# Optimization experiments

Hardware: AMD Instinct MI355X
Metric: run time of the kernel (lower is better)

Reference implementation:

```python
import jax, jax.numpy as jnp
import numpy as np

EPS = 1e-6
NEG_SLOPE = 0.2


def knn_idx(xf, k):
    # xf: (B, C, N) flattened vector features; returns (B, N, k) neighbor indices
    xx = jnp.sum(xf * xf, axis=1)                       # (B, N)
    inner = jnp.einsum('bcn,bcm->bnm', xf, xf)          # (B, N, N)
    neg_dist = 2.0 * inner - xx[:, :, None] - xx[:, None, :]  # -||xi-xj||^2
    _, idx = jax.lax.top_k(neg_dist, k)                 # includes self (dist 0)
    return idx


def get_graph_feature(x, k):
    # x: (B, D, 3, N) -> edge features (B, 2D, 3, N, k)
    B, D, _, N = x.shape
    idx = knn_idx(x.reshape(B, D * 3, N), k)            # (B, N, k)
    pts = jnp.transpose(x, (0, 3, 1, 2))                # (B, N, D, 3)
    neigh = jax.vmap(lambda p, i: p[i])(pts, idx)       # (B, N, k, D, 3) gather
    center = jnp.broadcast_to(pts[:, :, None], neigh.shape)
    feat = jnp.concatenate([neigh - center, center], axis=3)  # (B, N, k, 2D, 3)
    return jnp.transpose(feat, (0, 3, 4, 1, 2))


def vn_linear_leakyrelu(x, Wf, Wd):
    # Vector-Neuron linear + leaky ReLU. x: (B, Cin, 3, ...),
    # Wf: (Cout, Cin), Wd: (Cout, Cin) or (1, Cin) when nonlinearity is shared.
    p = jnp.einsum('oi,bi...->bo...', Wf, x)
    d = jnp.einsum('oi,bi...->bo...', Wd, x)
    dot = jnp.sum(p * d, axis=2, keepdims=True)
    dsq = jnp.sum(d * d, axis=2, keepdims=True)
    proj = p - (dot / (dsq + EPS)) * d
    return NEG_SLOPE * p + (1.0 - NEG_SLOPE) * jnp.where(dot >= 0, p, proj)


def setup_inputs() -> dict:
    key = jax.random.key(0)
    ks = jax.random.split(key, 11)
    B, N = 8, 1024
    x = jax.random.normal(ks[0], (B, 3, N), dtype=jnp.float32)
    # dims = [1, 21, 21, 42, 85, 341]
    ins = [2, 42, 42, 84, 169]      # 2*dim_in for edge layers; sum(dims[1:-1]) for last
    outs = [21, 21, 42, 85, 341]
    dirs = [21, 21, 42, 85, 1]      # last layer has share_nonlinearity=True
    d = {"x": x}
    for i, (ci, co, cd) in enumerate(zip(ins, outs, dirs)):
        s = 1.0 / np.sqrt(ci)
        kf, kd = jax.random.split(ks[1 + i])
        d[f"Wf{i}"] = (jax.random.normal(kf, (co, ci), dtype=jnp.float32) * s)
        d[f"Wd{i}"] = (jax.random.normal(kd, (cd, ci), dtype=jnp.float32) * s)
    d["k"] = 20
    return d


def reference(x, Wf0, Wd0, Wf1, Wd1, Wf2, Wd2, Wf3, Wd3, Wf4, Wd4, k):
    cur = x[:, None]                 # (B, 1, 3, N)
    feats = []
    for Wf, Wd in ((Wf0, Wd0), (Wf1, Wd1), (Wf2, Wd2), (Wf3, Wd3)):
        g = get_graph_feature(cur, k)        # (B, 2D, 3, N, k)
        h = vn_linear_leakyrelu(g, Wf, Wd)   # (B, Dout, 3, N, k)
        cur = h.mean(axis=-1)                # mean over neighbors -> (B, Dout, 3, N)
        feats.append(cur)
    xcat = jnp.concatenate(feats, axis=1)    # (B, 169, 3, N)
    out = vn_linear_leakyrelu(xcat, Wf4, Wd4)
    return out.mean(axis=-1)                 # mean over points -> (B, 341, 3)
```

## Files before the change

kernel.cpp:

```cpp
#include <hip/hip_runtime.h>
#include <cstddef>

#define BB 8
#define NN 1024
#define KK 20
#define CCAT 169
#define NT 16

__global__ __launch_bounds__(256) void dist_tile_kernel(
    const float* __restrict__ src, int bs, int F, float* __restrict__ dist) {
  __shared__ float As[8][128];
  __shared__ float Bs[8][128];
  int b = blockIdx.z;
  int n0 = blockIdx.y * 128;
  int m0 = blockIdx.x * 128;
  int t = threadIdx.x;
  int tx = t & 15, ty = t >> 4;
  const float* p = src + (size_t)b * bs;

  float acc[8][8];
  float xn[8], xm[8];
#pragma unroll
  for (int i = 0; i < 8; ++i) {
    xn[i] = 0.f;
    xm[i] = 0.f;
#pragma unroll
    for (int j = 0; j < 8; ++j) acc[i][j] = 0.f;
  }

  int fr = t >> 5;
  int cc = (t & 31) << 2;
  for (int f0 = 0; f0 < F; f0 += 8) {
    int f = f0 + fr;
    float4 av = {0.f, 0.f, 0.f, 0.f}, bv = {0.f, 0.f, 0.f, 0.f};
    if (f < F) {
      av = *(const float4*)(p + (size_t)f * NN + n0 + cc);
      bv = *(const float4*)(p + (size_t)f * NN + m0 + cc);
    }
    __syncthreads();
    *(float4*)&As[fr][cc] = av;
    *(float4*)&Bs[fr][cc] = bv;
    __syncthreads();
#pragma unroll
    for (int f2 = 0; f2 < 8; ++f2) {
      float4 al = *(const float4*)&As[f2][ty << 2];
      float4 ah = *(const float4*)&As[f2][64 + (ty << 2)];
      float4 bl = *(const float4*)&Bs[f2][tx << 2];
      float4 bh = *(const float4*)&Bs[f2][64 + (tx << 2)];
      float a[8] = {al.x, al.y, al.z, al.w, ah.x, ah.y, ah.z, ah.w};
      float bb[8] = {bl.x, bl.y, bl.z, bl.w, bh.x, bh.y, bh.z, bh.w};
#pragma unroll
      for (int i = 0; i < 8; ++i) xn[i] += a[i] * a[i];
#pragma unroll
      for (int j = 0; j < 8; ++j) xm[j] += bb[j] * bb[j];
#pragma unroll
      for (int i = 0; i < 8; ++i)
#pragma unroll
        for (int j = 0; j < 8; ++j) acc[i][j] += a[i] * bb[j];
    }
  }

#pragma unroll
  for (int i = 0; i < 8; ++i) {
    int n = n0 + ((i < 4) ? ((ty << 2) + i) : (64 + (ty << 2) + i - 4));
    float* dr = dist + (((size_t)b * NN + n) << 10);
    float4 w0, w1;
    w0.x = 2.f * acc[i][0] - xn[i] - xm[0];
    w0.y = 2.f * acc[i][1] - xn[i] - xm[1];
    w0.z = 2.f * acc[i][2] - xn[i] - xm[2];
    w0.w = 2.f * acc[i][3] - xn[i] - xm[3];
    w1.x = 2.f * acc[i][4] - xn[i] - xm[4];
    w1.y = 2.f * acc[i][5] - xn[i] - xm[5];
    w1.z = 2.f * acc[i][6] - xn[i] - xm[6];
    w1.w = 2.f * acc[i][7] - xn[i] - xm[7];
    *(float4*)(dr + m0 + (tx << 2)) = w0;
    *(float4*)(dr + m0 + 64 + (tx << 2)) = w1;
  }
}

__device__ __forceinline__ unsigned long long shfl_xor_u64(
    unsigned long long v, int off) {
  unsigned lo = (unsigned)v, hi = (unsigned)(v >> 32);
  lo = __shfl_xor(lo, off, 64);
  hi = __shfl_xor(hi, off, 64);
  return ((unsigned long long)hi << 32) | lo;
}

__global__ __launch_bounds__(256) void topk_kernel(
    const float* __restrict__ dist, int* __restrict__ idx_out) {
  int wave = threadIdx.x >> 6;
  int lane = threadIdx.x & 63;
  int row = blockIdx.x * 4 + wave;
  const float* d = dist + ((size_t)row << 10);

  unsigned long long key[16];
#pragma unroll
  for (int s = 0; s < 16; ++s) {
    int m = lane + (s << 6);
    unsigned u = __float_as_uint(d[m]);
    u = (u & 0x80000000u) ? ~u : (u | 0x80000000u);
    key[s] = ((unsigned long long)u << 32) | (unsigned)(NN - 1 - m);
  }

#pragma unroll
  for (int size = 2; size <= 16; size <<= 1) {
#pragma unroll
    for (int stride = size >> 1; stride > 0; stride >>= 1) {
#pragma unroll
      for (int i = 0; i < 16; ++i) {
        int j = i ^ stride;
        if (j > i) {
          unsigned long long a = key[i], c = key[j];
          bool desc = ((i & size) == 0);
          bool sw = desc ? (a < c) : (a > c);
          key[i] = sw ? c : a;
          key[j] = sw ? a : c;
        }
      }
    }
  }

  int* out = idx_out + row * KK;
  unsigned long long head = key[0];
  for (int r = 0; r < KK; ++r) {
    unsigned long long w = head;
#pragma unroll
    for (int off = 32; off > 0; off >>= 1) {
      unsigned long long o = shfl_xor_u64(w, off);
      if (o > w) w = o;
    }
    if (lane == 0) out[r] = (NN - 1) - (int)(w & 0xFFFFFFFFull);
    if (head == w) {
#pragma unroll
      for (int s = 0; s < 15; ++s) key[s] = key[s + 1];
      key[15] = 0ull;
      head = key[0];
    }
  }
}

__global__ __launch_bounds__(256) void edge_fused_kernel(
    const float* __restrict__ src, int bs, int D, int Co,
    const float* __restrict__ Wf, const float* __restrict__ Wd,
    const int* __restrict__ idx, int ooff, float* __restrict__ xcat) {
  __shared__ float2 Ulds[3 * NN];
  __shared__ float2 Vlds[3 * NN];
  __shared__ float4 Wlds[48];
  int bo = blockIdx.x;
  int b = bo / Co, o = bo % Co;
  int t = threadIdx.x;

  if (t < D) {
    float wfa = Wf[o * 2 * D + t];
    float wfb = Wf[o * 2 * D + D + t] - wfa;
    float wda = Wd[o * 2 * D + t];
    float wdb = Wd[o * 2 * D + D + t] - wda;
    Wlds[t] = make_float4(wfa, wfb, wda, wdb);
  }
  __syncthreads();

  const float* sb = src + (size_t)b * bs;
#pragma unroll
  for (int r = 0; r < 3; ++r) {
    int g = t + 256 * r;
    float4 uf = {0.f, 0.f, 0.f, 0.f}, vf = {0.f, 0.f, 0.f, 0.f};
    float4 ud = {0.f, 0.f, 0.f, 0.f}, vd = {0.f, 0.f, 0.f, 0.f};
    for (int i = 0; i < D; ++i) {
      float4 s = *(const float4*)(sb + (size_t)i * 3 * NN + (g << 2));
      float4 w = Wlds[i];
      uf.x += w.x * s.x; uf.y += w.x * s.y; uf.z += w.x * s.z; uf.w += w.x * s.w;
      vf.x += w.y * s.x; vf.y += w.y * s.y; vf.z += w.y * s.z; vf.w += w.y * s.w;
      ud.x += w.z * s.x; ud.y += w.z * s.y; ud.z += w.z * s.z; ud.w += w.z * s.w;
      vd.x += w.w * s.x; vd.y += w.w * s.y; vd.z += w.w * s.z; vd.w += w.w * s.w;
    }
    *(float4*)&Ulds[(g << 2) + 0] = make_float4(uf.x, ud.x, uf.y, ud.y);
    *(float4*)&Ulds[(g << 2) + 2] = make_float4(uf.z, ud.z, uf.w, ud.w);
    *(float4*)&Vlds[(g << 2) + 0] = make_float4(vf.x, vd.x, vf.y, vd.y);
    *(float4*)&Vlds[(g << 2) + 2] = make_float4(vf.z, vd.z, vf.w, vd.w);
  }
  __syncthreads();

  const float inv_k = 1.f / KK;
#pragma unroll
  for (int rep = 0; rep < 4; ++rep) {
    int n = rep * 256 + t;
    float2 v0 = Vlds[n];
    float2 v1 = Vlds[NN + n];
    float2 v2 = Vlds[2 * NN + n];
    const int4* ip = (const int4*)(idx + (b * NN + n) * KK);
    float a0 = 0.f, a1 = 0.f, a2 = 0.f;
#pragma unroll
    for (int q = 0; q < 5; ++q) {
      int4 iv = ip[q];
      int nbs[4] = {iv.x, iv.y, iv.z, iv.w};
#pragma unroll
      for (int jj = 0; jj < 4; ++jj) {
        int nb = nbs[jj];
        float2 u0 = Ulds[nb];
        float2 u1 = Ulds[NN + nb];
        float2 u2 = Ulds[2 * NN + nb];
        float pf0 = u0.x + v0.x, pd0 = u0.y + v0.y;
        float pf1 = u1.x + v1.x, pd1 = u1.y + v1.y;
        float pf2 = u2.x + v2.x, pd2 = u2.y + v2.y;
        float dot = pf0 * pd0 + pf1 * pd1 + pf2 * pd2;
        float dsq = pd0 * pd0 + pd1 * pd1 + pd2 * pd2;
        float g = (dot >= 0.f) ? 0.f : 0.8f * dot / (dsq + 1e-6f);
        a0 += pf0 - g * pd0;
        a1 += pf1 - g * pd1;
        a2 += pf2 - g * pd2;
      }
    }
    size_t ob = (size_t)b * CCAT * 3 * NN + (size_t)(ooff + o) * 3 * NN + n;
    xcat[ob] = a0 * inv_k;
    xcat[ob + NN] = a1 * inv_k;
    xcat[ob + 2 * NN] = a2 * inv_k;
  }
}

__global__ __launch_bounds__(256) void final_fused_kernel(
    const float* __restrict__ xcat, const float* __restrict__ Wf4,
    const float* __restrict__ Wd4, float* __restrict__ part) {
  __shared__ float Ws[2][16][64];
  __shared__ float Xs[2][3][16][64];
  __shared__ float Wds[2][16];
  int b = blockIdx.z;
  int o0 = blockIdx.y * 64;
  int n0 = blockIdx.x * 64;
  int t = threadIdx.x;
  int tx = t & 15, ty = t >> 4;
  int ow = t & 63, fq = t >> 6;

  float acc[3][4][4];
  float dv[3][4];
#pragma unroll
  for (int c = 0; c < 3; ++c) {
#pragma unroll
    for (int i = 0; i < 4; ++i)
#pragma unroll
      for (int j = 0; j < 4; ++j) acc[c][i][j] = 0.f;
#pragma unroll
    for (int j = 0; j < 4; ++j) dv[c][j] = 0.f;
  }

  const float* xb = xcat + (size_t)b * CCAT * 3 * NN;
  const int NTILE = (CCAT + 15) / 16;

  float4 xv[3];
  float wreg[4];
  float wdv;

  auto stage = [&](int tt) {
    int f = tt * 16 + ty;
#pragma unroll
    for (int c = 0; c < 3; ++c) {
      xv[c] = make_float4(0.f, 0.f, 0.f, 0.f);
      if (f < CCAT)
        xv[c] = *(const float4*)(xb + ((size_t)f * 3 + c) * NN + n0 + (tx << 2));
    }
    int o = o0 + ow;
#pragma unroll
    for (int e = 0; e < 4; ++e) {
      int fw = tt * 16 + (fq << 2) + e;
      wreg[e] = (o < 341 && fw < CCAT) ? Wf4[(size_t)o * CCAT + fw] : 0.f;
    }
    wdv = 0.f;
    if (t < 16) {
      int fd = tt * 16 + t;
      if (fd < CCAT) wdv = Wd4[fd];
    }
  };
  auto store = [&](int buf) {
#pragma unroll
    for (int c = 0; c < 3; ++c) *(float4*)&Xs[buf][c][ty][tx << 2] = xv[c];
#pragma unroll
    for (int e = 0; e < 4; ++e) Ws[buf][(fq << 2) + e][ow] = wreg[e];
    if (t < 16) Wds[buf][t] = wdv;
  };

  stage(0);
  store(0);

  for (int tt = 0; tt < NTILE; ++tt) {
    int buf = tt & 1;
    __syncthreads();
    if (tt + 1 < NTILE) stage(tt + 1);
#pragma unroll
    for (int f2 = 0; f2 < 16; ++f2) {
      float4 w = *(const float4*)&Ws[buf][f2][ty << 2];
      float wa[4] = {w.x, w.y, w.z, w.w};
      float wd = Wds[buf][f2];
#pragma unroll
      for (int c = 0; c < 3; ++c) {
        float4 x = *(const float4*)&Xs[buf][c][f2][tx << 2];
        float xa[4] = {x.x, x.y, x.z, x.w};
#pragma unroll
        for (int j = 0; j < 4; ++j) dv[c][j] += wd * xa[j];
#pragma unroll
        for (int i = 0; i < 4; ++i)
#pragma unroll
          for (int j = 0; j < 4; ++j) acc[c][i][j] += wa[i] * xa[j];
      }
    }
    if (tt + 1 < NTILE) store(buf ^ 1);
  }

  float s[3][4];
#pragma unroll
  for (int c = 0; c < 3; ++c)
#pragma unroll
    for (int i = 0; i < 4; ++i) s[c][i] = 0.f;
#pragma unroll
  for (int i = 0; i < 4; ++i) {
#pragma unroll
    for (int j = 0; j < 4; ++j) {
      float d0 = dv[0][j], d1 = dv[1][j], d2 = dv[2][j];
      float p0 = acc[0][i][j], p1 = acc[1][i][j], p2 = acc[2][i][j];
      float dot = p0 * d0 + p1 * d1 + p2 * d2;
      float dsq = d0 * d0 + d1 * d1 + d2 * d2;
      float g = (dot >= 0.f) ? 0.f : 0.8f * dot / (dsq + 1e-6f);
      s[0][i] += p0 - g * d0;
      s[1][i] += p1 - g * d1;
      s[2][i] += p2 - g * d2;
    }
  }

#pragma unroll
  for (int off = 1; off < 16; off <<= 1) {
#pragma unroll
    for (int c = 0; c < 3; ++c)
#pragma unroll
      for (int i = 0; i < 4; ++i) s[c][i] += __shfl_xor(s[c][i], off, 64);
  }
  if (tx == 0) {
#pragma unroll
    for (int i = 0; i < 4; ++i) {
      int o = o0 + (ty << 2) + i;
      if (o < 341) {
#pragma unroll
        for (int c = 0; c < 3; ++c)
          part[(((size_t)b * 341 + o) * 3 + c) * NT + blockIdx.x] = s[c][i];
      }
    }
  }
}

__global__ void final_reduce_kernel(const float* __restrict__ part,
                                    float* __restrict__ out) {
  int t = blockIdx.x * 256 + threadIdx.x;
  if (t >= BB * 341 * 3) return;
  const float* p = part + (size_t)t * NT;
  float s = 0.f;
#pragma unroll
  for (int nt = 0; nt < NT; ++nt) s += p[nt];
  out[t] = s * (1.f / 1024.f);
}

extern "C" void kernel_launch(void* const* d_in, const int* in_sizes, int n_in,
                              void* d_out, int out_size, void* d_ws,
                              size_t ws_size, hipStream_t stream) {
  (void)in_sizes; (void)n_in; (void)out_size; (void)ws_size;
  const float* x = (const float*)d_in[0];
  const float* Wf[5] = {(const float*)d_in[1], (const float*)d_in[3],
                        (const float*)d_in[5], (const float*)d_in[7],
                        (const float*)d_in[9]};
  const float* Wd[5] = {(const float*)d_in[2], (const float*)d_in[4],
                        (const float*)d_in[6], (const float*)d_in[8],
                        (const float*)d_in[10]};

  float* ws = (float*)d_ws;
  float* dist = ws;
  float* part = ws;
  size_t off = (size_t)BB * NN * NN;
  int* idx = (int*)(ws + off);
  off += (size_t)BB * NN * KK;
  float* xcat = ws + off;

  struct LayerCfg { int D, Co, inoff, ooff; };
  const LayerCfg L[4] = {
      {1, 21, 0, 0},
      {21, 21, 0, 21},
      {21, 42, 21, 42},
      {42, 85, 42, 84},
  };

  for (int l = 0; l < 4; ++l) {
    const float* src = (l == 0) ? x : (xcat + (size_t)L[l].inoff * 3 * NN);
    int bs = (l == 0) ? 3 * NN : CCAT * 3 * NN;
    int D = L[l].D, Co = L[l].Co;

    dist_tile_kernel<<<dim3(8, 8, BB), 256, 0, stream>>>(src, bs, 3 * D, dist);
    topk_kernel<<<(BB * NN) / 4, 256, 0, stream>>>(dist, idx);
    edge_fused_kernel<<<BB * Co, 256, 0, stream>>>(src, bs, D, Co, Wf[l],
                                                   Wd[l], idx, L[l].ooff,
                                                   xcat);
  }

  final_fused_kernel<<<dim3(NT, 6, BB), 256, 0, stream>>>(xcat, Wf[4], Wd[4],
                                                          part);
  final_reduce_kernel<<<(BB * 341 * 3 + 255) / 256, 256, 0, stream>>>(
      part, (float*)d_out);
}
```

Baseline: 467.5 us.

## Exploit distance matrix symmetry and restructure final layer tiling

The distance kernel now computes only upper-triangular 128x128 tiles (36 of 64 per batch) and writes each off-diagonal tile twice, once transposed, which removes nearly half of the Gram-matrix arithmetic. The transposed stores are strided per thread and so less coalesced. The final fused kernel replaces register double-buffering with a 32-wide single-buffered tile and preloads Wd4 into shared memory once. It also reorganises the Wf4 loads so each thread fetches four outputs for one feature.

```diff
diff --git a/kernel.cpp b/kernel.cpp
--- a/kernel.cpp
+++ b/kernel.cpp
@@ -12,8 +12,11 @@
   __shared__ float As[8][128];
   __shared__ float Bs[8][128];
   int b = blockIdx.z;
-  int n0 = blockIdx.y * 128;
-  int m0 = blockIdx.x * 128;
+  int rem = blockIdx.x, bi = 0;
+  while (rem >= 8 - bi) { rem -= 8 - bi; ++bi; }
+  int bj = bi + rem;
+  int n0 = bi * 128;
+  int m0 = bj * 128;
   int t = threadIdx.x;
   int tx = t & 15, ty = t >> 4;
   const float* p = src + (size_t)b * bs;
@@ -61,20 +64,30 @@
   }
 
 #pragma unroll
+  for (int i = 0; i < 8; ++i)
+#pragma unroll
+    for (int j = 0; j < 8; ++j) acc[i][j] = 2.f * acc[i][j] - xn[i] - xm[j];
+
+#pragma unroll
   for (int i = 0; i < 8; ++i) {
     int n = n0 + ((i < 4) ? ((ty << 2) + i) : (64 + (ty << 2) + i - 4));
     float* dr = dist + (((size_t)b * NN + n) << 10);
-    float4 w0, w1;
-    w0.x = 2.f * acc[i][0] - xn[i] - xm[0];
-    w0.y = 2.f * acc[i][1] - xn[i] - xm[1];
-    w0.z = 2.f * acc[i][2] - xn[i] - xm[2];
-    w0.w = 2.f * acc[i][3] - xn[i] - xm[3];
-    w1.x = 2.f * acc[i][4] - xn[i] - xm[4];
-    w1.y = 2.f * acc[i][5] - xn[i] - xm[5];
-    w1.z = 2.f * acc[i][6] - xn[i] - xm[6];
-    w1.w = 2.f * acc[i][7] - xn[i] - xm[7];
-    *(float4*)(dr + m0 + (tx << 2)) = w0;
-    *(float4*)(dr + m0 + 64 + (tx << 2)) = w1;
+    *(float4*)(dr + m0 + (tx << 2)) =
+        make_float4(acc[i][0], acc[i][1], acc[i][2], acc[i][3]);
+    *(float4*)(dr + m0 + 64 + (tx << 2)) =
+        make_float4(acc[i][4], acc[i][5], acc[i][6], acc[i][7]);
+  }
+
+  if (bi != bj) {
+#pragma unroll
+    for (int j = 0; j < 8; ++j) {
+      int m = m0 + ((j < 4) ? ((tx << 2) + j) : (64 + (tx << 2) + j - 4));
+      float* dr = dist + (((size_t)b * NN + m) << 10);
+      *(float4*)(dr + n0 + (ty << 2)) =
+          make_float4(acc[0][j], acc[1][j], acc[2][j], acc[3][j]);
+      *(float4*)(dr + n0 + 64 + (ty << 2)) =
+          make_float4(acc[4][j], acc[5][j], acc[6][j], acc[7][j]);
+    }
   }
 }
 
@@ -220,15 +233,16 @@
 __global__ __launch_bounds__(256) void final_fused_kernel(
     const float* __restrict__ xcat, const float* __restrict__ Wf4,
     const float* __restrict__ Wd4, float* __restrict__ part) {
-  __shared__ float Ws[2][16][64];
-  __shared__ float Xs[2][3][16][64];
-  __shared__ float Wds[2][16];
+  __shared__ float Ws[32][64];
+  __shared__ float Xs[3][32][64];
+  __shared__ float Wda[192];
   int b = blockIdx.z;
   int o0 = blockIdx.y * 64;
   int n0 = blockIdx.x * 64;
   int t = threadIdx.x;
   int tx = t & 15, ty = t >> 4;
-  int ow = t & 63, fq = t >> 6;
+
+  if (t < 192) Wda[t] = (t < CCAT) ? Wd4[t] : 0.f;
 
   float acc[3][4][4];
   float dv[3][4];
@@ -243,55 +257,45 @@
   }
 
   const float* xb = xcat + (size_t)b * CCAT * 3 * NN;
-  const int NTILE = (CCAT + 15) / 16;
-
-  float4 xv[3];
-  float wreg[4];
-  float wdv;
-
-  auto stage = [&](int tt) {
-    int f = tt * 16 + ty;
-#pragma unroll
-    for (int c = 0; c < 3; ++c) {
-      xv[c] = make_float4(0.f, 0.f, 0.f, 0.f);
-      if (f < CCAT)
-        xv[c] = *(const float4*)(xb + ((size_t)f * 3 + c) * NN + n0 + (tx << 2));
-    }
-    int o = o0 + ow;
-#pragma unroll
-    for (int e = 0; e < 4; ++e) {
-      int fw = tt * 16 + (fq << 2) + e;
-      wreg[e] = (o < 341 && fw < CCAT) ? Wf4[(size_t)o * CCAT + fw] : 0.f;
-    }
-    wdv = 0.f;
-    if (t < 16) {
-      int fd = tt * 16 + t;
-      if (fd < CCAT) wdv = Wd4[fd];
-    }
-  };
-  auto store = [&](int buf) {
-#pragma unroll
-    for (int c = 0; c < 3; ++c) *(float4*)&Xs[buf][c][ty][tx << 2] = xv[c];
-#pragma unroll
-    for (int e = 0; e < 4; ++e) Ws[buf][(fq << 2) + e][ow] = wreg[e];
-    if (t < 16) Wds[buf][t] = wdv;
-  };
-
-  stage(0);
-  store(0);
+  const int NTILE = (CCAT + 31) / 32;
 
   for (int tt = 0; tt < NTILE; ++tt) {
-    int buf = tt & 1;
+    float4 xv[2][3];
+    float wv[2][4];
+#pragma unroll
+    for (int r = 0; r < 2; ++r) {
+      int f = tt * 32 + r * 16 + ty;
+#pragma unroll
+      for (int c = 0; c < 3; ++c) {
+        xv[r][c] = make_float4(0.f, 0.f, 0.f, 0.f);
+        if (f < CCAT)
+          xv[r][c] =
+              *(const float4*)(xb + ((size_t)f * 3 + c) * NN + n0 + (tx << 2));
+      }
+#pragma unroll
+      for (int q = 0; q < 4; ++q) {
+        int o = o0 + (tx << 2) + q;
+        wv[r][q] = (o < 341 && f < CCAT) ? Wf4[(size_t)o * CCAT + f] : 0.f;
+      }
+    }
     __syncthreads();
-    if (tt + 1 < NTILE) stage(tt + 1);
-#pragma unroll
-    for (int f2 = 0; f2 < 16; ++f2) {
-      float4 w = *(const float4*)&Ws[buf][f2][ty << 2];
+#pragma unroll
+    for (int r = 0; r < 2; ++r) {
+#pragma unroll
+      for (int c = 0; c < 3; ++c)
+        *(float4*)&Xs[c][r * 16 + ty][tx << 2] = xv[r][c];
+      *(float4*)&Ws[r * 16 + ty][tx << 2] =
+          make_float4(wv[r][0], wv[r][1], wv[r][2], wv[r][3]);
+    }
+    __syncthreads();
+#pragma unroll
+    for (int f2 = 0; f2 < 32; ++f2) {
+      float4 w = *(const float4*)&Ws[f2][ty << 2];
       float wa[4] = {w.x, w.y, w.z, w.w};
-      float wd = Wds[buf][f2];
+      float wd = Wda[tt * 32 + f2];
 #pragma unroll
       for (int c = 0; c < 3; ++c) {
-        float4 x = *(const float4*)&Xs[buf][c][f2][tx << 2];
+        float4 x = *(const float4*)&Xs[c][f2][tx << 2];
         float xa[4] = {x.x, x.y, x.z, x.w};
 #pragma unroll
         for (int j = 0; j < 4; ++j) dv[c][j] += wd * xa[j];
@@ -301,7 +305,6 @@
           for (int j = 0; j < 4; ++j) acc[c][i][j] += wa[i] * xa[j];
       }
     }
-    if (tt + 1 < NTILE) store(buf ^ 1);
   }
 
   float s[3][4];
@@ -388,7 +391,7 @@
     int bs = (l == 0) ? 3 * NN : CCAT * 3 * NN;
     int D = L[l].D, Co = L[l].Co;
 
-    dist_tile_kernel<<<dim3(8, 8, BB), 256, 0, stream>>>(src, bs, 3 * D, dist);
+    dist_tile_kernel<<<dim3(36, 1, BB), 256, 0, stream>>>(src, bs, 3 * D, dist);
     topk_kernel<<<(BB * NN) / 4, 256, 0, stream>>>(dist, idx);
     edge_fused_kernel<<<BB * Co, 256, 0, stream>>>(src, bs, D, Co, Wf[l],
                                                    Wd[l], idx, L[l].ooff,
```

Result: faster. 451.4 us (-3.4%).
